# Performance work log

Hardware: AMD Instinct MI355X
Metric: run time of the kernel (lower is better)

The kernel has to match this reference:

```python
import jax, jax.numpy as jnp
import numpy as np

NUM_ITER = 2
B, NS, NK = 64, 11, 4096
QI = KVI = QKO = VO = 128
LN_EPS = 1e-5
ATTN_EPS = 1e-8


def setup_inputs() -> dict:
    key = jax.random.key(0)
    ks = jax.random.split(key, 20)
    rn = lambda i, shp, sc: jax.random.normal(ks[i], shp, jnp.float32) * sc
    d = {
        "query": rn(0, (B, NS, QI), 1.0),
        "inputs": rn(1, (B, NK, KVI), 1.0),
        # LayerNorm params
        "ln_q_g": jnp.ones((QI,), jnp.float32),
        "ln_q_b": jnp.zeros((QI,), jnp.float32),
        "ln_kv_g": jnp.ones((KVI,), jnp.float32),
        "ln_kv_b": jnp.zeros((KVI,), jnp.float32),
        # projections (stored [in, out]; torch Linear weight transposed)
        "Wq": rn(2, (QI, QKO), QI ** -0.5),
        "Wk": rn(3, (KVI, QKO), KVI ** -0.5),
        "Wv": rn(4, (KVI, VO), KVI ** -0.5),
        # GRU cell params
        "W_ir": rn(5, (VO, VO), VO ** -0.5),
        "b_ir": jnp.zeros((VO,), jnp.float32),
        "W_iz": rn(6, (VO, VO), VO ** -0.5),
        "b_iz": jnp.zeros((VO,), jnp.float32),
        "W_hr": rn(7, (VO, VO), VO ** -0.5),
        "W_hz": rn(8, (VO, VO), VO ** -0.5),
        "W_in": rn(9, (VO, VO), VO ** -0.5),
        "b_in": jnp.zeros((VO,), jnp.float32),
        "W_hn": rn(10, (VO, VO), VO ** -0.5),
        "b_hn": jnp.zeros((VO,), jnp.float32),
    }
    return d


def _layernorm(x, g, b):
    mu = x.mean(-1, keepdims=True)
    var = ((x - mu) ** 2).mean(-1, keepdims=True)  # biased var, matches torch LN
    return (x - mu) * jax.lax.rsqrt(var + LN_EPS) * g + b


def reference(query, inputs, ln_q_g, ln_q_b, ln_kv_g, ln_kv_b, Wq, Wk, Wv,
              W_ir, b_ir, W_iz, b_iz, W_hr, W_hz, W_in, b_in, W_hn, b_hn):
    x = _layernorm(inputs, ln_kv_g, ln_kv_b)          # [b, nk, kvi]
    k = x @ Wk                                        # [b, nk, qko]
    v = x @ Wv                                        # [b, nk, vo]
    scale = 1.0 / jnp.sqrt(jnp.float32(Wq.shape[1]))
    for _ in range(NUM_ITER):
        q = _layernorm(query, ln_q_g, ln_q_b) @ Wq    # [b, ns, qko]
        q = q * scale
        # inverted SDPA: softmax over slot axis m, renormalize over key axis n
        a = jax.nn.softmax(jnp.einsum('bmc,bnc->bmn', q, k), axis=1)
        a = a / (a.sum(axis=2, keepdims=True) + ATTN_EPS)
        upd = jnp.einsum('bmn,bnc->bmc', a, v)        # [b, ns, vo]
        # GRU cell update (per-slot)
        r = jax.nn.sigmoid(upd @ W_ir + b_ir + query @ W_hr)
        z = jax.nn.sigmoid(upd @ W_iz + b_iz + query @ W_hz)
        n = jnp.tanh(upd @ W_in + b_in + r * (query @ W_hn + b_hn))
        query = (1.0 - z) * n + z * query
    return query
```

## Files before the change

### kernel.cpp

```cpp
#include <hip/hip_runtime.h>
#include <hip/hip_bf16.h>


#define NKEYS 4096

typedef short short8 __attribute__((ext_vector_type(8)));
typedef float f32x4 __attribute__((ext_vector_type(4)));

__device__ __forceinline__ unsigned short f2bf(float x) {
    unsigned u = __float_as_uint(x);
    u += 0x7fffu + ((u >> 16) & 1u);
    return (unsigned short)(u >> 16);
}

__device__ __forceinline__ int xoff(int n, int cb) {
    return n * 256 + (cb ^ ((n & 7) << 4) ^ (((n >> 3) & 3) << 5));
}

__device__ __forceinline__ void gll16(const void* g, void* l) {
    __builtin_amdgcn_global_load_lds(
        (const __attribute__((address_space(1))) unsigned int*)g,
        (__attribute__((address_space(3))) unsigned int*)l, 16, 0, 0);
}

__global__ void kqq(const float* __restrict__ query, const float* __restrict__ g,
                    const float* __restrict__ be, const float* __restrict__ Wq,
                    const float* __restrict__ Wk, char* __restrict__ qfrag,
                    float* __restrict__ yz, float* __restrict__ dz) {
    int bm = blockIdx.x;
    int b = bm / 11, m = bm - b * 11;
    int c = threadIdx.x;
    yz[(b * 16 + m) * 128 + c] = 0.f;
    if (c == 0) dz[b * 16 + m] = 0.f;
    __shared__ float xs[128], qs[128];
    __shared__ float red[4];
    float x = query[bm * 128 + c];
    float s = x, ss = x * x;
#pragma unroll
    for (int mask = 1; mask < 64; mask <<= 1) {
        s += __shfl_xor(s, mask);
        ss += __shfl_xor(ss, mask);
    }
    int wid = threadIdx.x >> 6;
    if ((threadIdx.x & 63) == 0) { red[wid] = s; red[2 + wid] = ss; }
    __syncthreads();
    s = red[0] + red[1]; ss = red[2] + red[3];
    float mean = s * (1.f / 128.f);
    float var = ss * (1.f / 128.f) - mean * mean;
    float rstd = rsqrtf(var + 1e-5f);
    xs[c] = (x - mean) * rstd * g[c] + be[c];
    __syncthreads();
    float acc = 0.f;
#pragma unroll 8
    for (int k = 0; k < 128; k++) acc += xs[k] * Wq[k * 128 + c];
    qs[c] = acc * 0.088388347648318447f;
    __syncthreads();
    const float4* wr = (const float4*)(Wk + c * 128);
    float qk = 0.f;
#pragma unroll 8
    for (int k4 = 0; k4 < 32; k4++) {
        float4 wv = wr[k4];
        qk += qs[k4 * 4] * wv.x + qs[k4 * 4 + 1] * wv.y +
              qs[k4 * 4 + 2] * wv.z + qs[k4 * 4 + 3] * wv.w;
    }
    int kc = c >> 5, hi = (c >> 3) & 3, j = c & 7;
    *(unsigned short*)(qfrag + b * 4096 + kc * 1024 + (hi * 16 + m) * 16 + j * 2) = f2bf(qk);
}

__global__ __launch_bounds__(256) void kf(
    const float* __restrict__ inputs, const float* __restrict__ gkv,
    const float* __restrict__ bkv, const char* __restrict__ qfrag,
    char* __restrict__ kg, float* __restrict__ yacc, float* __restrict__ dacc_g) {
    __shared__ __align__(16) char smem[18432];
    const int PO = 16384;
    int tid = threadIdx.x;
    int b = blockIdx.x >> 4, gt = blockIdx.x & 15;
    int w = tid >> 6, lane = tid & 63, hi = lane >> 4, lo = lane & 15;
    int a_ = tid >> 5, col4 = tid & 31;

    short8 qa[4];
#pragma unroll
    for (int kc = 0; kc < 4; kc++)
        qa[kc] = *(const short8*)(qfrag + b * 4096 + kc * 1024 + lane * 16);

    float4 g4  = *(const float4*)(gkv + col4 * 4);
    float4 be4 = *(const float4*)(bkv + col4 * 4);

    f32x4 y0 = {0, 0, 0, 0}, y1 = {0, 0, 0, 0};
    float dr[4] = {0, 0, 0, 0};

    const float4* inp4 = (const float4*)(inputs + ((size_t)b * NKEYS + gt * 256) * 128);

    float4 xa[8];
#pragma unroll
    for (int i = 0; i < 8; i++) xa[i] = inp4[tid + 256 * i];

#pragma unroll
    for (int t = 0; t < 4; t++) {
        float4 xb[8];
        if (t < 3) {
#pragma unroll
            for (int i = 0; i < 8; i++) xb[i] = inp4[(t + 1) * 2048 + tid + 256 * i];
        }
        size_t tb = ((size_t)(b * 64 + gt * 4 + t)) * 16384;
#pragma unroll
        for (int i = 0; i < 8; i++) {
            float4 xv = xa[i];
            int row = a_ + 8 * i;
            float s = xv.x + xv.y + xv.z + xv.w;
            float ss = xv.x * xv.x + xv.y * xv.y + xv.z * xv.z + xv.w * xv.w;
#pragma unroll
            for (int mask = 1; mask < 32; mask <<= 1) {
                s += __shfl_xor(s, mask);
                ss += __shfl_xor(ss, mask);
            }
            float mean = s * (1.f / 128.f);
            float var = ss * (1.f / 128.f) - mean * mean;
            float rstd = rsqrtf(var + 1e-5f);
            unsigned short h0 = f2bf((xv.x - mean) * rstd * g4.x + be4.x);
            unsigned short h1 = f2bf((xv.y - mean) * rstd * g4.y + be4.y);
            unsigned short h2 = f2bf((xv.z - mean) * rstd * g4.z + be4.z);
            unsigned short h3 = f2bf((xv.w - mean) * rstd * g4.w + be4.w);
            uint2 pk;
            pk.x = (unsigned)h0 | ((unsigned)h1 << 16);
            pk.y = (unsigned)h2 | ((unsigned)h3 << 16);
            int off = xoff(row, col4 * 8);
            *(uint2*)(smem + off) = pk;
            *(uint2*)(kg + tb + off) = pk;
        }
        asm volatile("s_waitcnt lgkmcnt(0)" ::: "memory");
        __builtin_amdgcn_s_barrier();
        __builtin_amdgcn_sched_barrier(0);

        f32x4 lacc = {0, 0, 0, 0};
        int n = w * 16 + lo;
#pragma unroll
        for (int kc = 0; kc < 4; kc++) {
            short8 kf8 = *(short8*)(smem + xoff(n, kc * 64 + hi * 16));
            lacc = __builtin_amdgcn_mfma_f32_16x16x32_bf16(qa[kc], kf8, lacc, 0, 0, 0);
        }
        float mx = -1e30f;
#pragma unroll
        for (int r = 0; r < 4; r++) {
            int m = hi * 4 + r;
            mx = fmaxf(mx, (m < 11) ? lacc[r] : -1e30f);
        }
        mx = fmaxf(mx, __shfl_xor(mx, 16));
        mx = fmaxf(mx, __shfl_xor(mx, 32));
        float p[4]; float s = 0.f;
#pragma unroll
        for (int r = 0; r < 4; r++) {
            int m = hi * 4 + r;
            p[r] = (m < 11) ? __expf(lacc[r] - mx) : 0.f;
            s += p[r];
        }
        s += __shfl_xor(s, 16);
        s += __shfl_xor(s, 32);
        float inv = 1.f / s;
#pragma unroll
        for (int r = 0; r < 4; r++) {
            p[r] *= inv;
            dr[r] += p[r];
            int m = hi * 4 + r;
            *(unsigned short*)(smem + PO + m * 128 + (((w * 16 + lo) * 2) ^ ((m & 7) << 4))) =
                f2bf(p[r]);
        }
        asm volatile("s_waitcnt lgkmcnt(0)" ::: "memory");
        __builtin_amdgcn_s_barrier();
        __builtin_amdgcn_sched_barrier(0);

#pragma unroll
        for (int s2 = 0; s2 < 2; s2++) {
            short8 pf = *(short8*)(smem + PO + lo * 128 + ((s2 * 64 + hi * 16) ^ ((lo & 7) << 4)));
            short8 v0, v1;
#pragma unroll
            for (int j = 0; j < 8; j++) {
                int nn = s2 * 32 + hi * 8 + j;
                v0[j] = *(short*)(smem + xoff(nn, (w * 32 + lo) * 2));
                v1[j] = *(short*)(smem + xoff(nn, (w * 32 + 16 + lo) * 2));
            }
            y0 = __builtin_amdgcn_mfma_f32_16x16x32_bf16(pf, v0, y0, 0, 0, 0);
            y1 = __builtin_amdgcn_mfma_f32_16x16x32_bf16(pf, v1, y1, 0, 0, 0);
        }
        asm volatile("s_waitcnt lgkmcnt(0)" ::: "memory");
        __builtin_amdgcn_s_barrier();
        __builtin_amdgcn_sched_barrier(0);
        if (t < 3) {
#pragma unroll
            for (int i = 0; i < 8; i++) xa[i] = xb[i];
        }
    }

#pragma unroll
    for (int r = 0; r < 4; r++) {
        int m = hi * 4 + r;
        if (m < 11) {
            atomicAdd(&yacc[(b * 16 + m) * 128 + w * 32 + lo], y0[r]);
            atomicAdd(&yacc[(b * 16 + m) * 128 + w * 32 + 16 + lo], y1[r]);
        }
    }
#pragma unroll
    for (int mask = 1; mask < 16; mask <<= 1) {
#pragma unroll
        for (int r = 0; r < 4; r++) dr[r] += __shfl_xor(dr[r], mask);
    }
    if (lo == 0) {
#pragma unroll
        for (int r = 0; r < 4; r++) {
            int m = hi * 4 + r;
            if (m < 11) atomicAdd(&dacc_g[b * 16 + m], dr[r]);
        }
    }
}

__global__ __launch_bounds__(256) void kb(
    const char* __restrict__ kg, const char* __restrict__ qfrag,
    float* __restrict__ yacc, float* __restrict__ dacc_g) {
    __shared__ __align__(16) char smem[34816];
    const int PO = 32768;
    int tid = threadIdx.x;
    int b = blockIdx.x >> 4, gt = blockIdx.x & 15;
    int w = tid >> 6, lane = tid & 63, hi = lane >> 4, lo = lane & 15;

    short8 qa[4];
#pragma unroll
    for (int kc = 0; kc < 4; kc++)
        qa[kc] = *(const short8*)(qfrag + b * 4096 + kc * 1024 + lane * 16);

    f32x4 y0 = {0, 0, 0, 0}, y1 = {0, 0, 0, 0};
    float dr[4] = {0, 0, 0, 0};

    size_t base = ((size_t)(b * 64 + gt * 4)) * 16384;
    int reg = w * 4096;

#pragma unroll
    for (int j = 0; j < 4; j++) {
        int o = reg + j * 1024;
        gll16(kg + base + o + lane * 16, smem + o);
    }

#pragma unroll
    for (int t = 0; t < 4; t++) {
        int XB = (t & 1) * 16384;
        asm volatile("s_waitcnt vmcnt(0)" ::: "memory");
        __builtin_amdgcn_s_barrier();
        __builtin_amdgcn_sched_barrier(0);
        if (t < 3) {
            size_t tbn = base + (size_t)(t + 1) * 16384;
            int nb = ((t + 1) & 1) * 16384;
#pragma unroll
            for (int j = 0; j < 4; j++) {
                int o = reg + j * 1024;
                gll16(kg + tbn + o + lane * 16, smem + nb + o);
            }
        }

        f32x4 lacc = {0, 0, 0, 0};
        int n = w * 16 + lo;
#pragma unroll
        for (int kc = 0; kc < 4; kc++) {
            short8 kf8 = *(short8*)(smem + XB + xoff(n, kc * 64 + hi * 16));
            lacc = __builtin_amdgcn_mfma_f32_16x16x32_bf16(qa[kc], kf8, lacc, 0, 0, 0);
        }
        float mx = -1e30f;
#pragma unroll
        for (int r = 0; r < 4; r++) {
            int m = hi * 4 + r;
            mx = fmaxf(mx, (m < 11) ? lacc[r] : -1e30f);
        }
        mx = fmaxf(mx, __shfl_xor(mx, 16));
        mx = fmaxf(mx, __shfl_xor(mx, 32));
        float p[4]; float s = 0.f;
#pragma unroll
        for (int r = 0; r < 4; r++) {
            int m = hi * 4 + r;
            p[r] = (m < 11) ? __expf(lacc[r] - mx) : 0.f;
            s += p[r];
        }
        s += __shfl_xor(s, 16);
        s += __shfl_xor(s, 32);
        float inv = 1.f / s;
#pragma unroll
        for (int r = 0; r < 4; r++) {
            p[r] *= inv;
            dr[r] += p[r];
            int m = hi * 4 + r;
            *(unsigned short*)(smem + PO + m * 128 + (((w * 16 + lo) * 2) ^ ((m & 7) << 4))) =
                f2bf(p[r]);
        }
        asm volatile("s_waitcnt lgkmcnt(0)" ::: "memory");
        __builtin_amdgcn_s_barrier();
        __builtin_amdgcn_sched_barrier(0);

#pragma unroll
        for (int s2 = 0; s2 < 2; s2++) {
            short8 pf = *(short8*)(smem + PO + lo * 128 + ((s2 * 64 + hi * 16) ^ ((lo & 7) << 4)));
            short8 v0, v1;
#pragma unroll
            for (int j = 0; j < 8; j++) {
                int nn = s2 * 32 + hi * 8 + j;
                v0[j] = *(short*)(smem + XB + xoff(nn, (w * 32 + lo) * 2));
                v1[j] = *(short*)(smem + XB + xoff(nn, (w * 32 + 16 + lo) * 2));
            }
            y0 = __builtin_amdgcn_mfma_f32_16x16x32_bf16(pf, v0, y0, 0, 0, 0);
            y1 = __builtin_amdgcn_mfma_f32_16x16x32_bf16(pf, v1, y1, 0, 0, 0);
        }
        asm volatile("s_waitcnt lgkmcnt(0)" ::: "memory");
        __builtin_amdgcn_sched_barrier(0);
    }

#pragma unroll
    for (int r = 0; r < 4; r++) {
        int m = hi * 4 + r;
        if (m < 11) {
            atomicAdd(&yacc[(b * 16 + m) * 128 + w * 32 + lo], y0[r]);
            atomicAdd(&yacc[(b * 16 + m) * 128 + w * 32 + 16 + lo], y1[r]);
        }
    }
#pragma unroll
    for (int mask = 1; mask < 16; mask <<= 1) {
#pragma unroll
        for (int r = 0; r < 4; r++) dr[r] += __shfl_xor(dr[r], mask);
    }
    if (lo == 0) {
#pragma unroll
        for (int r = 0; r < 4; r++) {
            int m = hi * 4 + r;
            if (m < 11) atomicAdd(&dacc_g[b * 16 + m], dr[r]);
        }
    }
}

__global__ void kun(const float* __restrict__ yacc, const float* __restrict__ dacc,
                    const float* __restrict__ qcur, const float* __restrict__ Wv,
                    const float* __restrict__ W_ir, const float* __restrict__ b_ir,
                    const float* __restrict__ W_iz, const float* __restrict__ b_iz,
                    const float* __restrict__ W_hr, const float* __restrict__ W_hz,
                    const float* __restrict__ W_in, const float* __restrict__ b_in,
                    const float* __restrict__ W_hn, const float* __restrict__ b_hn,
                    float* __restrict__ qnext, int mode,
                    const float* __restrict__ lqg, const float* __restrict__ lqb,
                    const float* __restrict__ Wq, const float* __restrict__ Wk,
                    char* __restrict__ qfrag, float* __restrict__ yz,
                    float* __restrict__ dz) {
    int bm = blockIdx.x;
    int b = bm / 11, m = bm % 11;
    int c = threadIdx.x;
    __shared__ float ys[128], us[128], qs[128];
    __shared__ float red[4];
    float den = dacc[b * 16 + m] + 1e-8f;
    ys[c] = yacc[(b * 16 + m) * 128 + c] / den;
    qs[c] = qcur[bm * 128 + c];
    __syncthreads();
    float upd = 0.f;
#pragma unroll 4
    for (int k = 0; k < 128; k++) upd += ys[k] * Wv[k * 128 + c];
    us[c] = upd;
    __syncthreads();
    float air = 0, aiz = 0, ain = 0, ahr = 0, ahz = 0, ahn = 0;
#pragma unroll 4
    for (int k = 0; k < 128; k++) {
        float u = us[k], q = qs[k];
        air += u * W_ir[k * 128 + c];
        aiz += u * W_iz[k * 128 + c];
        ain += u * W_in[k * 128 + c];
        ahr += q * W_hr[k * 128 + c];
        ahz += q * W_hz[k * 128 + c];
        ahn += q * W_hn[k * 128 + c];
    }
    float r = 1.f / (1.f + expf(-(air + b_ir[c] + ahr)));
    float z = 1.f / (1.f + expf(-(aiz + b_iz[c] + ahz)));
    float n = tanhf(ain + b_in[c] + r * (ahn + b_hn[c]));
    float qn = (1.f - z) * n + z * qs[c];
    qnext[bm * 128 + c] = qn;
    if (mode == 0) return;
    yz[(b * 16 + m) * 128 + c] = 0.f;
    if (c == 0) dz[b * 16 + m] = 0.f;
    float s = qn, ss = qn * qn;
#pragma unroll
    for (int mask = 1; mask < 64; mask <<= 1) {
        s += __shfl_xor(s, mask);
        ss += __shfl_xor(ss, mask);
    }
    int wid = c >> 6;
    if ((c & 63) == 0) { red[wid] = s; red[2 + wid] = ss; }
    __syncthreads();
    s = red[0] + red[1]; ss = red[2] + red[3];
    float mean = s * (1.f / 128.f);
    float var = ss * (1.f / 128.f) - mean * mean;
    float rstd = rsqrtf(var + 1e-5f);
    ys[c] = (qn - mean) * rstd * lqg[c] + lqb[c];
    __syncthreads();
    float acc = 0.f;
#pragma unroll 8
    for (int k = 0; k < 128; k++) acc += ys[k] * Wq[k * 128 + c];
    us[c] = acc * 0.088388347648318447f;
    __syncthreads();
    const float4* wr = (const float4*)(Wk + c * 128);
    float qk = 0.f;
#pragma unroll 8
    for (int k4 = 0; k4 < 32; k4++) {
        float4 wv = wr[k4];
        qk += us[k4 * 4] * wv.x + us[k4 * 4 + 1] * wv.y +
              us[k4 * 4 + 2] * wv.z + us[k4 * 4 + 3] * wv.w;
    }
    int kc = c >> 5, hi = (c >> 3) & 3, j = c & 7;
    *(unsigned short*)(qfrag + b * 4096 + kc * 1024 + (hi * 16 + m) * 16 + j * 2) = f2bf(qk);
}

__global__ void kq(const float* __restrict__ query, const float* __restrict__ g,
                   const float* __restrict__ be, const float* __restrict__ Wq,
                   float* __restrict__ qout) {
    int bm = blockIdx.x;
    int c = threadIdx.x;
    __shared__ float xs[128];
    __shared__ float red[4];
    float x = query[bm * 128 + c];
    float s = x, ss = x * x;
#pragma unroll
    for (int mask = 1; mask < 64; mask <<= 1) {
        s += __shfl_xor(s, mask);
        ss += __shfl_xor(ss, mask);
    }
    int wid = threadIdx.x >> 6;
    if ((threadIdx.x & 63) == 0) { red[wid] = s; red[2 + wid] = ss; }
    __syncthreads();
    s = red[0] + red[1]; ss = red[2] + red[3];
    float mean = s * (1.f / 128.f);
    float var = ss * (1.f / 128.f) - mean * mean;
    float rstd = rsqrtf(var + 1e-5f);
    xs[c] = (x - mean) * rstd * g[c] + be[c];
    __syncthreads();
    float acc = 0.f;
#pragma unroll 8
    for (int k = 0; k < 128; k++) acc += xs[k] * Wq[k * 128 + c];
    qout[bm * 128 + c] = acc * 0.088388347648318447f;
}

__global__ __launch_bounds__(256) void ks(
    const float* __restrict__ inputs, const float* __restrict__ gkv,
    const float* __restrict__ bkv, const float* __restrict__ Wk,
    const float* __restrict__ Wv, const float* __restrict__ qbuf,
    float* __restrict__ upd_acc, float* __restrict__ d_acc) {
    __shared__ __align__(16) char smem[51200];
    const int XO = 0, KO = 16384, VB = 32768, PO = 49152;

    int tid = threadIdx.x;
    int b = blockIdx.x >> 4, g = blockIdx.x & 15;
    int w = tid >> 6, lane = tid & 63, hi = lane >> 4, lo = lane & 15;

    short8 bk[2][4], bv[2][4];
#pragma unroll
    for (int ct = 0; ct < 2; ct++) {
        int col = w * 32 + ct * 16 + lo;
#pragma unroll
        for (int kc = 0; kc < 4; kc++) {
            short8 fk, fv;
#pragma unroll
            for (int j = 0; j < 8; j++) {
                int rr = kc * 32 + hi * 8 + j;
                fk[j] = (short)f2bf(Wk[rr * 128 + col]);
                fv[j] = (short)f2bf(Wv[rr * 128 + col]);
            }
            bk[ct][kc] = fk; bv[ct][kc] = fv;
        }
    }
    short8 qa[4];
#pragma unroll
    for (int kc = 0; kc < 4; kc++) {
        short8 f;
#pragma unroll
        for (int j = 0; j < 8; j++)
            f[j] = (lo < 11) ? (short)f2bf(qbuf[(b * 11 + lo) * 128 + kc * 32 + hi * 8 + j])
                             : (short)0;
        qa[kc] = f;
    }
    int col4 = tid & 31;
    float4 g4  = *(const float4*)(gkv + col4 * 4);
    float4 be4 = *(const float4*)(bkv + col4 * 4);

    f32x4 uacc0 = {0, 0, 0, 0}, uacc1 = {0, 0, 0, 0};
    float dacc[4] = {0, 0, 0, 0};

    const float4* inp4 = (const float4*)(inputs + ((size_t)b * NKEYS + g * 256) * 128);
    int a_ = tid >> 5;

    for (int t = 0; t < 4; t++) {
#pragma unroll
        for (int i = 0; i < 8; i++) {
            int f = tid + 256 * i;
            float4 xv = inp4[t * 2048 + f];
            int row = a_ + 8 * i;
            float s = xv.x + xv.y + xv.z + xv.w;
            float ss = xv.x * xv.x + xv.y * xv.y + xv.z * xv.z + xv.w * xv.w;
#pragma unroll
            for (int mask = 1; mask < 32; mask <<= 1) {
                s += __shfl_xor(s, mask);
                ss += __shfl_xor(ss, mask);
            }
            float mean = s * (1.f / 128.f);
            float var = ss * (1.f / 128.f) - mean * mean;
            float rstd = rsqrtf(var + 1e-5f);
            unsigned short h0 = f2bf((xv.x - mean) * rstd * g4.x + be4.x);
            unsigned short h1 = f2bf((xv.y - mean) * rstd * g4.y + be4.y);
            unsigned short h2 = f2bf((xv.z - mean) * rstd * g4.z + be4.z);
            unsigned short h3 = f2bf((xv.w - mean) * rstd * g4.w + be4.w);
            uint2 pk;
            pk.x = (unsigned)h0 | ((unsigned)h1 << 16);
            pk.y = (unsigned)h2 | ((unsigned)h3 << 16);
            int byte = row * 256 + ((col4 * 8) ^ ((row & 7) << 4));
            *(uint2*)(smem + XO + byte) = pk;
        }
        __syncthreads();
#pragma unroll
        for (int mt = 0; mt < 4; mt++) {
            f32x4 ka0 = {0,0,0,0}, ka1 = {0,0,0,0}, va0 = {0,0,0,0}, va1 = {0,0,0,0};
            int arow = mt * 16 + lo;
#pragma unroll
            for (int kc = 0; kc < 4; kc++) {
                int abyte = arow * 256 + ((kc * 64 + hi * 16) ^ ((arow & 7) << 4));
                short8 af = *(short8*)(smem + XO + abyte);
                ka0 = __builtin_amdgcn_mfma_f32_16x16x32_bf16(af, bk[0][kc], ka0, 0, 0, 0);
                ka1 = __builtin_amdgcn_mfma_f32_16x16x32_bf16(af, bk[1][kc], ka1, 0, 0, 0);
                va0 = __builtin_amdgcn_mfma_f32_16x16x32_bf16(af, bv[0][kc], va0, 0, 0, 0);
                va1 = __builtin_amdgcn_mfma_f32_16x16x32_bf16(af, bv[1][kc], va1, 0, 0, 0);
            }
#pragma unroll
            for (int r = 0; r < 4; r++) {
                int n = mt * 16 + hi * 4 + r;
                int c0 = w * 32 + lo;
                int c1 = c0 + 16;
                *(unsigned short*)(smem + KO + n * 256 + ((c0 * 2) ^ ((n & 7) << 4))) = f2bf(ka0[r]);
                *(unsigned short*)(smem + KO + n * 256 + ((c1 * 2) ^ ((n & 7) << 4))) = f2bf(ka1[r]);
                *(unsigned short*)(smem + VB + c0 * 128 + ((n * 2) ^ ((c0 & 7) << 4))) = f2bf(va0[r]);
                *(unsigned short*)(smem + VB + c1 * 128 + ((n * 2) ^ ((c1 & 7) << 4))) = f2bf(va1[r]);
            }
        }
        __syncthreads();
        {
            f32x4 lacc = {0, 0, 0, 0};
            int n = w * 16 + lo;
#pragma unroll
            for (int kc = 0; kc < 4; kc++) {
                int kbyte = n * 256 + ((kc * 64 + hi * 16) ^ ((n & 7) << 4));
                short8 kf8 = *(short8*)(smem + KO + kbyte);
                lacc = __builtin_amdgcn_mfma_f32_16x16x32_bf16(qa[kc], kf8, lacc, 0, 0, 0);
            }
            float mx = -1e30f;
#pragma unroll
            for (int r = 0; r < 4; r++) {
                int m = hi * 4 + r;
                float v = (m < 11) ? lacc[r] : -1e30f;
                mx = fmaxf(mx, v);
            }
            mx = fmaxf(mx, __shfl_xor(mx, 16));
            mx = fmaxf(mx, __shfl_xor(mx, 32));
            float p[4]; float s = 0.f;
#pragma unroll
            for (int r = 0; r < 4; r++) {
                int m = hi * 4 + r;
                p[r] = (m < 11) ? __expf(lacc[r] - mx) : 0.f;
                s += p[r];
            }
            s += __shfl_xor(s, 16);
            s += __shfl_xor(s, 32);
            float inv = 1.f / s;
#pragma unroll
            for (int r = 0; r < 4; r++) {
                p[r] *= inv;
                dacc[r] += p[r];
                int m = hi * 4 + r;
                *(unsigned short*)(smem + PO + m * 128 + (((w * 16 + lo) * 2) ^ ((m & 7) << 4))) =
                    f2bf(p[r]);
            }
        }
        __syncthreads();
#pragma unroll
        for (int kc2 = 0; kc2 < 2; kc2++) {
            int pbyte = lo * 128 + ((kc2 * 64 + hi * 16) ^ ((lo & 7) << 4));
            short8 pf = *(short8*)(smem + PO + pbyte);
            int c0 = w * 32 + lo;
            int vb0 = c0 * 128 + ((kc2 * 64 + hi * 16) ^ ((c0 & 7) << 4));
            short8 vf0 = *(short8*)(smem + VB + vb0);
            uacc0 = __builtin_amdgcn_mfma_f32_16x16x32_bf16(pf, vf0, uacc0, 0, 0, 0);
            int c1 = c0 + 16;
            int vb1 = c1 * 128 + ((kc2 * 64 + hi * 16) ^ ((c1 & 7) << 4));
            short8 vf1 = *(short8*)(smem + VB + vb1);
            uacc1 = __builtin_amdgcn_mfma_f32_16x16x32_bf16(pf, vf1, uacc1, 0, 0, 0);
        }
    }
#pragma unroll
    for (int r = 0; r < 4; r++) {
        int m = hi * 4 + r;
        if (m < 11) {
            atomicAdd(&upd_acc[(b * 16 + m) * 128 + w * 32 + lo], uacc0[r]);
            atomicAdd(&upd_acc[(b * 16 + m) * 128 + w * 32 + 16 + lo], uacc1[r]);
        }
    }
#pragma unroll
    for (int mask = 1; mask < 16; mask <<= 1) {
#pragma unroll
        for (int r = 0; r < 4; r++) dacc[r] += __shfl_xor(dacc[r], mask);
    }
    if (lo == 0) {
#pragma unroll
        for (int r = 0; r < 4; r++) {
            int m = hi * 4 + r;
            if (m < 11) atomicAdd(&d_acc[b * 16 + m], dacc[r]);
        }
    }
}

__global__ void ku(const float* __restrict__ upd_acc, const float* __restrict__ d_acc,
                   const float* __restrict__ qcur,
                   const float* __restrict__ W_ir, const float* __restrict__ b_ir,
                   const float* __restrict__ W_iz, const float* __restrict__ b_iz,
                   const float* __restrict__ W_hr, const float* __restrict__ W_hz,
                   const float* __restrict__ W_in, const float* __restrict__ b_in,
                   const float* __restrict__ W_hn, const float* __restrict__ b_hn,
                   float* __restrict__ qnext) {
    int bm = blockIdx.x;
    int b = bm / 11, m = bm % 11;
    int c = threadIdx.x;
    __shared__ float us[128], qs[128];
    float den = d_acc[b * 16 + m] + 1e-8f;
    us[c] = upd_acc[(b * 16 + m) * 128 + c] / den;
    qs[c] = qcur[bm * 128 + c];
    __syncthreads();
    float air = 0, aiz = 0, ain = 0, ahr = 0, ahz = 0, ahn = 0;
#pragma unroll 4
    for (int k = 0; k < 128; k++) {
        float u = us[k], q = qs[k];
        air += u * W_ir[k * 128 + c];
        aiz += u * W_iz[k * 128 + c];
        ain += u * W_in[k * 128 + c];
        ahr += q * W_hr[k * 128 + c];
        ahz += q * W_hz[k * 128 + c];
        ahn += q * W_hn[k * 128 + c];
    }
    float r = 1.f / (1.f + expf(-(air + b_ir[c] + ahr)));
    float z = 1.f / (1.f + expf(-(aiz + b_iz[c] + ahz)));
    float n = tanhf(ain + b_in[c] + r * (ahn + b_hn[c]));
    qnext[bm * 128 + c] = (1.f - z) * n + z * qs[c];
}

extern "C" void kernel_launch(void* const* d_in, const int* in_sizes, int n_in,
                              void* d_out, int out_size, void* d_ws, size_t ws_size,
                              hipStream_t stream) {
    const float* query   = (const float*)d_in[0];
    const float* inputs  = (const float*)d_in[1];
    const float* ln_q_g  = (const float*)d_in[2];
    const float* ln_q_b  = (const float*)d_in[3];
    const float* ln_kv_g = (const float*)d_in[4];
    const float* ln_kv_b = (const float*)d_in[5];
    const float* Wq      = (const float*)d_in[6];
    const float* Wk      = (const float*)d_in[7];
    const float* Wv      = (const float*)d_in[8];
    const float* W_ir    = (const float*)d_in[9];
    const float* b_ir    = (const float*)d_in[10];
    const float* W_iz    = (const float*)d_in[11];
    const float* b_iz    = (const float*)d_in[12];
    const float* W_hr    = (const float*)d_in[13];
    const float* W_hz    = (const float*)d_in[14];
    const float* W_in    = (const float*)d_in[15];
    const float* b_in    = (const float*)d_in[16];
    const float* W_hn    = (const float*)d_in[17];
    const float* b_hn    = (const float*)d_in[18];

    char* ws = (char*)d_ws;
    float* query_buf = (float*)(ws);
    float* yacc      = (float*)(ws + 360448);
    float* dacc      = (float*)(ws + 884736);
    char*  qfrag     = ws + 888832;
    char*  kg        = ws + 1150976;
    const size_t need = 1150976ull + 67108864ull;

    if (ws_size >= need) {
        kqq<<<704, 128, 0, stream>>>(query, ln_q_g, ln_q_b, Wq, Wk, qfrag, yacc, dacc);
        kf<<<1024, 256, 0, stream>>>(inputs, ln_kv_g, ln_kv_b, qfrag, kg, yacc, dacc);
        kun<<<704, 128, 0, stream>>>(yacc, dacc, query, Wv,
                                     W_ir, b_ir, W_iz, b_iz, W_hr, W_hz,
                                     W_in, b_in, W_hn, b_hn, query_buf, 1,
                                     ln_q_g, ln_q_b, Wq, Wk, qfrag, yacc, dacc);
        kb<<<1024, 256, 0, stream>>>(kg, qfrag, yacc, dacc);
        kun<<<704, 128, 0, stream>>>(yacc, dacc, query_buf, Wv,
                                     W_ir, b_ir, W_iz, b_iz, W_hr, W_hz,
                                     W_in, b_in, W_hn, b_hn, (float*)d_out, 0,
                                     ln_q_g, ln_q_b, Wq, Wk, qfrag, yacc, dacc);
    } else {
        float* q_buf = (float*)(ws + 888832);
        const float* cur = query;
        for (int it = 0; it < 2; it++) {
            kq<<<704, 128, 0, stream>>>(cur, ln_q_g, ln_q_b, Wq, q_buf);
            hipMemsetAsync(ws + 360448, 0, 524288 + 4096, stream);
            ks<<<1024, 256, 0, stream>>>(inputs, ln_kv_g, ln_kv_b, Wk, Wv, q_buf, yacc, dacc);
            float* qn = (it == 0) ? query_buf : (float*)d_out;
            ku<<<704, 128, 0, stream>>>(yacc, dacc, cur,
                                        W_ir, b_ir, W_iz, b_iz, W_hr, W_hz,
                                        W_in, b_in, W_hn, b_hn, qn);
            cur = query_buf;
        }
    }
}
```

Baseline: 145.0 us.

## Permute bf16 feature layout in LDS so V reads use paired 32-bit loads

Changes how normalized key/value features are packed in shared memory and the key cache. Each thread now handles columns c and c+16 together and stores them interleaved, so the value-side MFMA operand gathers read one 32-bit word feeding both output tiles instead of two 16-bit loads. The query fragment layout is permuted to match the new channel order, and the LayerNorm reduction shrinks to 16-lane shuffles with 128-bit stores. It also adds an occupancy hint to launch bounds, which may constrain register allocation.

```diff
diff --git a/kernel.cpp b/kernel.cpp
--- a/kernel.cpp
+++ b/kernel.cpp
@@ -63,11 +63,11 @@
         qk += qs[k4 * 4] * wv.x + qs[k4 * 4 + 1] * wv.y +
               qs[k4 * 4 + 2] * wv.z + qs[k4 * 4 + 3] * wv.w;
     }
-    int kc = c >> 5, hi = (c >> 3) & 3, j = c & 7;
+    int kc = c >> 5, hi = (c >> 2) & 3, j = 2 * (c & 3) + ((c >> 4) & 1);
     *(unsigned short*)(qfrag + b * 4096 + kc * 1024 + (hi * 16 + m) * 16 + j * 2) = f2bf(qk);
 }
 
-__global__ __launch_bounds__(256) void kf(
+__global__ __launch_bounds__(256, 4) void kf(
     const float* __restrict__ inputs, const float* __restrict__ gkv,
     const float* __restrict__ bkv, const char* __restrict__ qfrag,
     char* __restrict__ kg, float* __restrict__ yacc, float* __restrict__ dacc_g) {
@@ -76,57 +76,72 @@
     int tid = threadIdx.x;
     int b = blockIdx.x >> 4, gt = blockIdx.x & 15;
     int w = tid >> 6, lane = tid & 63, hi = lane >> 4, lo = lane & 15;
-    int a_ = tid >> 5, col4 = tid & 31;
+    int r0 = tid >> 4;
+    int bq = (tid >> 2) & 3;
+    int tq = tid & 3;
+    int cb0 = bq * 32 + tq * 4;
 
     short8 qa[4];
 #pragma unroll
     for (int kc = 0; kc < 4; kc++)
         qa[kc] = *(const short8*)(qfrag + b * 4096 + kc * 1024 + lane * 16);
 
-    float4 g4  = *(const float4*)(gkv + col4 * 4);
-    float4 be4 = *(const float4*)(bkv + col4 * 4);
+    float4 gx0 = *(const float4*)(gkv + cb0);
+    float4 gx1 = *(const float4*)(gkv + cb0 + 16);
+    float4 bx0 = *(const float4*)(bkv + cb0);
+    float4 bx1 = *(const float4*)(bkv + cb0 + 16);
 
     f32x4 y0 = {0, 0, 0, 0}, y1 = {0, 0, 0, 0};
     float dr[4] = {0, 0, 0, 0};
 
-    const float4* inp4 = (const float4*)(inputs + ((size_t)b * NKEYS + gt * 256) * 128);
-
-    float4 xa[8];
-#pragma unroll
-    for (int i = 0; i < 8; i++) xa[i] = inp4[tid + 256 * i];
+    const float* xsrc = inputs + ((size_t)b * NKEYS + gt * 256) * 128;
+
+    float4 xa0[4], xa1[4];
+#pragma unroll
+    for (int i = 0; i < 4; i++) {
+        int row = r0 + 16 * i;
+        xa0[i] = *(const float4*)(xsrc + row * 128 + cb0);
+        xa1[i] = *(const float4*)(xsrc + row * 128 + cb0 + 16);
+    }
 
 #pragma unroll
     for (int t = 0; t < 4; t++) {
-        float4 xb[8];
+        float4 xb0[4], xb1[4];
         if (t < 3) {
 #pragma unroll
-            for (int i = 0; i < 8; i++) xb[i] = inp4[(t + 1) * 2048 + tid + 256 * i];
+            for (int i = 0; i < 4; i++) {
+                int row = (t + 1) * 64 + r0 + 16 * i;
+                xb0[i] = *(const float4*)(xsrc + row * 128 + cb0);
+                xb1[i] = *(const float4*)(xsrc + row * 128 + cb0 + 16);
+            }
         }
         size_t tb = ((size_t)(b * 64 + gt * 4 + t)) * 16384;
 #pragma unroll
-        for (int i = 0; i < 8; i++) {
-            float4 xv = xa[i];
-            int row = a_ + 8 * i;
-            float s = xv.x + xv.y + xv.z + xv.w;
-            float ss = xv.x * xv.x + xv.y * xv.y + xv.z * xv.z + xv.w * xv.w;
-#pragma unroll
-            for (int mask = 1; mask < 32; mask <<= 1) {
-                s += __shfl_xor(s, mask);
-                ss += __shfl_xor(ss, mask);
-            }
+        for (int i = 0; i < 4; i++) {
+            int row = r0 + 16 * i;
+            float4 v0 = xa0[i], v1 = xa1[i];
+            float s = v0.x + v0.y + v0.z + v0.w + v1.x + v1.y + v1.z + v1.w;
+            float ss = v0.x * v0.x + v0.y * v0.y + v0.z * v0.z + v0.w * v0.w +
+                       v1.x * v1.x + v1.y * v1.y + v1.z * v1.z + v1.w * v1.w;
+            s += __shfl_xor(s, 1); ss += __shfl_xor(ss, 1);
+            s += __shfl_xor(s, 2); ss += __shfl_xor(ss, 2);
+            s += __shfl_xor(s, 4); ss += __shfl_xor(ss, 4);
+            s += __shfl_xor(s, 8); ss += __shfl_xor(ss, 8);
             float mean = s * (1.f / 128.f);
             float var = ss * (1.f / 128.f) - mean * mean;
             float rstd = rsqrtf(var + 1e-5f);
-            unsigned short h0 = f2bf((xv.x - mean) * rstd * g4.x + be4.x);
-            unsigned short h1 = f2bf((xv.y - mean) * rstd * g4.y + be4.y);
-            unsigned short h2 = f2bf((xv.z - mean) * rstd * g4.z + be4.z);
-            unsigned short h3 = f2bf((xv.w - mean) * rstd * g4.w + be4.w);
-            uint2 pk;
-            pk.x = (unsigned)h0 | ((unsigned)h1 << 16);
-            pk.y = (unsigned)h2 | ((unsigned)h3 << 16);
-            int off = xoff(row, col4 * 8);
-            *(uint2*)(smem + off) = pk;
-            *(uint2*)(kg + tb + off) = pk;
+            uint4 qw;
+            qw.x = (unsigned)f2bf((v0.x - mean) * rstd * gx0.x + bx0.x) |
+                   ((unsigned)f2bf((v1.x - mean) * rstd * gx1.x + bx1.x) << 16);
+            qw.y = (unsigned)f2bf((v0.y - mean) * rstd * gx0.y + bx0.y) |
+                   ((unsigned)f2bf((v1.y - mean) * rstd * gx1.y + bx1.y) << 16);
+            qw.z = (unsigned)f2bf((v0.z - mean) * rstd * gx0.z + bx0.z) |
+                   ((unsigned)f2bf((v1.z - mean) * rstd * gx1.z + bx1.z) << 16);
+            qw.w = (unsigned)f2bf((v0.w - mean) * rstd * gx0.w + bx0.w) |
+                   ((unsigned)f2bf((v1.w - mean) * rstd * gx1.w + bx1.w) << 16);
+            int off = xoff(row, bq * 64 + tq * 16);
+            *(uint4*)(smem + off) = qw;
+            *(uint4*)(kg + tb + off) = qw;
         }
         asm volatile("s_waitcnt lgkmcnt(0)" ::: "memory");
         __builtin_amdgcn_s_barrier();
@@ -176,8 +191,9 @@
 #pragma unroll
             for (int j = 0; j < 8; j++) {
                 int nn = s2 * 32 + hi * 8 + j;
-                v0[j] = *(short*)(smem + xoff(nn, (w * 32 + lo) * 2));
-                v1[j] = *(short*)(smem + xoff(nn, (w * 32 + 16 + lo) * 2));
+                unsigned rd = *(unsigned*)(smem + xoff(nn, w * 64 + lo * 4));
+                v0[j] = (short)(rd & 0xffffu);
+                v1[j] = (short)(rd >> 16);
             }
             y0 = __builtin_amdgcn_mfma_f32_16x16x32_bf16(pf, v0, y0, 0, 0, 0);
             y1 = __builtin_amdgcn_mfma_f32_16x16x32_bf16(pf, v1, y1, 0, 0, 0);
@@ -187,7 +203,7 @@
         __builtin_amdgcn_sched_barrier(0);
         if (t < 3) {
 #pragma unroll
-            for (int i = 0; i < 8; i++) xa[i] = xb[i];
+            for (int i = 0; i < 4; i++) { xa0[i] = xb0[i]; xa1[i] = xb1[i]; }
         }
     }
 
@@ -299,8 +315,9 @@
 #pragma unroll
             for (int j = 0; j < 8; j++) {
                 int nn = s2 * 32 + hi * 8 + j;
-                v0[j] = *(short*)(smem + XB + xoff(nn, (w * 32 + lo) * 2));
-                v1[j] = *(short*)(smem + XB + xoff(nn, (w * 32 + 16 + lo) * 2));
+                unsigned rd = *(unsigned*)(smem + XB + xoff(nn, w * 64 + lo * 4));
+                v0[j] = (short)(rd & 0xffffu);
+                v1[j] = (short)(rd >> 16);
             }
             y0 = __builtin_amdgcn_mfma_f32_16x16x32_bf16(pf, v0, y0, 0, 0, 0);
             y1 = __builtin_amdgcn_mfma_f32_16x16x32_bf16(pf, v1, y1, 0, 0, 0);
@@ -404,7 +421,7 @@
         qk += us[k4 * 4] * wv.x + us[k4 * 4 + 1] * wv.y +
               us[k4 * 4 + 2] * wv.z + us[k4 * 4 + 3] * wv.w;
     }
-    int kc = c >> 5, hi = (c >> 3) & 3, j = c & 7;
+    int kc = c >> 5, hi = (c >> 2) & 3, j = 2 * (c & 3) + ((c >> 4) & 1);
     *(unsigned short*)(qfrag + b * 4096 + kc * 1024 + (hi * 16 + m) * 16 + j * 2) = f2bf(qk);
 }
 
```

New measurement: 160.3 us. 10.5% more time.
